# Optimization experiments

Hardware: AMD Instinct MI355X
Metric: run time of the kernel (lower is better)

Reference implementation:

```python
import jax, jax.numpy as jnp
import numpy as np

B, T, H = 1024, 1024, 64


def _lstm_cell(x, h, c, w_ih, w_hh, b_ih, b_hh):
    # gates: [B, 4H] in PyTorch order i, f, g, o
    g = x @ w_ih.T + h @ w_hh.T + b_ih + b_hh
    i, f, gg, o = jnp.split(g, 4, axis=-1)
    i = jax.nn.sigmoid(i)
    f = jax.nn.sigmoid(f)
    gg = jnp.tanh(gg)
    o = jax.nn.sigmoid(o)
    c_new = f * c + i * gg
    h_new = o * jnp.tanh(c_new)
    return h_new, c_new


def setup_inputs() -> dict:
    key = jax.random.key(0)
    ks = jax.random.split(key, 12)
    s = 1.0 / np.sqrt(H)  # torch default init scale
    r = lambda k, shape: jax.random.normal(k, shape, dtype=jnp.float32) * s
    return {
        "x": jax.random.normal(ks[0], (B, T), dtype=jnp.float32),
        "w_ih1": r(ks[1], (4 * H, 1)),
        "w_hh1": r(ks[2], (4 * H, H)),
        "b_ih1": r(ks[3], (4 * H,)),
        "b_hh1": r(ks[4], (4 * H,)),
        "w_ih2": r(ks[5], (4 * H, H)),
        "w_hh2": r(ks[6], (4 * H, H)),
        "b_ih2": r(ks[7], (4 * H,)),
        "b_hh2": r(ks[8], (4 * H,)),
        "w_lin": r(ks[9], (1, H)),
        "b_lin": r(ks[10], (1,)),
        "future_preds": 0,
    }


def reference(x, w_ih1, w_hh1, b_ih1, b_hh1, w_ih2, w_hh2, b_ih2, b_hh2,
              w_lin, b_lin, future_preds):
    bsz = x.shape[0]
    h1 = jnp.zeros((bsz, H), x.dtype)
    c1 = jnp.zeros((bsz, H), x.dtype)
    h2 = jnp.zeros((bsz, H), x.dtype)
    c2 = jnp.zeros((bsz, H), x.dtype)

    def step(carry, x_t):
        h1, c1, h2, c2 = carry
        h1, c1 = _lstm_cell(x_t, h1, c1, w_ih1, w_hh1, b_ih1, b_hh1)
        h2, c2 = _lstm_cell(h1, h2, c2, w_ih2, w_hh2, b_ih2, b_hh2)
        out = h2 @ w_lin.T + b_lin  # [B, 1]
        return (h1, c1, h2, c2), out

    xs = x.T[:, :, None]  # [T, B, 1]
    carry, outs = jax.lax.scan(step, (h1, c1, h2, c2), xs)
    outputs = outs[:, :, 0].T  # [B, T]

    if future_preds > 0:
        last = outs[-1]  # [B, 1]

        def fstep(carry, _):
            h1, c1, h2, c2, prev = carry
            h1, c1 = _lstm_cell(prev, h1, c1, w_ih1, w_hh1, b_ih1, b_hh1)
            h2, c2 = _lstm_cell(h1, h2, c2, w_ih2, w_hh2, b_ih2, b_hh2)
            out = h2 @ w_lin.T + b_lin
            return (h1, c1, h2, c2, out), out

        _, fouts = jax.lax.scan(fstep, (*carry, last), None, length=future_preds)
        outputs = jnp.concatenate([outputs, fouts[:, :, 0].T], axis=1)

    return outputs
```

## Files before the change

kernel.cpp:

```cpp
#include <hip/hip_runtime.h>
#include <hip/hip_bf16.h>


typedef _Float16 f16x8 __attribute__((ext_vector_type(8)));
typedef float    f32x4 __attribute__((ext_vector_type(4)));

namespace {
constexpr int Bb = 1024;
constexpr int Tt = 1024;
constexpr int NBat = 4;
constexpr int HSTR = 72;
constexpr int XSTR = 1025;

__device__ __forceinline__ int srow(int row) {
    return row ^ ((row >> 3) & 7);
}
__device__ __forceinline__ float sigm_pre(float a) {
    return __builtin_amdgcn_rcpf(1.0f + __builtin_amdgcn_exp2f(a));
}
__device__ __forceinline__ float tanh_pre(float a) {
    return fmaf(2.0f, __builtin_amdgcn_rcpf(1.0f + __builtin_amdgcn_exp2f(a)), -1.0f);
}
__device__ __forceinline__ float tanh_f(float x) {
    float e = __builtin_amdgcn_exp2f(-2.8853900817779268f * x);
    return fmaf(2.0f, __builtin_amdgcn_rcpf(1.0f + e), -1.0f);
}
template <int CTRL>
__device__ __forceinline__ float dpp_sum_step(float p) {
    int v = __builtin_amdgcn_update_dpp(0, __float_as_int(p), CTRL, 0xf, 0xf, true);
    return p + __int_as_float(v);
}
__device__ __forceinline__ bool detect_f32(const void* w) {
    const unsigned short* p = (const unsigned short*)w;
    int sane = 0;
    for (int i = 0; i < 64; ++i) {
        int e = (p[2 * i] >> 7) & 0xFF;
        if (e >= 107 && e <= 129) ++sane;
    }
    return sane < 32;
}
__device__ __forceinline__ float ld(const void* p, int i, bool f32) {
    return f32 ? ((const float*)p)[i]
               : __bfloat162float(((const __hip_bfloat16*)p)[i]);
}
__device__ __forceinline__ void st(void* p, int i, float v, bool f32) {
    if (f32) ((float*)p)[i] = v;
    else     ((__hip_bfloat16*)p)[i] = __float2bfloat16(v);
}
__device__ __forceinline__ void poll_flags(const int* f, int tp, int tq, int lane) {
    const int idx = lane & 7;
    const int thr = (idx < 4) ? tp : tq;
    for (;;) {
        int v = ((const volatile int*)f)[idx];
        if (__all(v >= thr)) break;
    }
    __builtin_amdgcn_sched_barrier(0);
    asm volatile("" ::: "memory");
}
}

__global__ __launch_bounds__(512, 1) void lstm2_kernel(
    const void* __restrict__ x,
    const void* __restrict__ w_ih1,
    const void* __restrict__ w_hh1,
    const void* __restrict__ b_ih1,
    const void* __restrict__ b_hh1,
    const void* __restrict__ w_ih2,
    const void* __restrict__ w_hh2,
    const void* __restrict__ b_ih2,
    const void* __restrict__ b_hh2,
    const void* __restrict__ w_lin,
    const void* __restrict__ b_lin,
    void* __restrict__ out)
{
    const int tid  = threadIdx.x;
    const int lane = tid & 63;
    const int w    = tid >> 6;
    const int gw   = w & 3;
    const bool isP = w < 4;
    const int m    = lane & 15;
    const int quad = lane >> 4;
    const int bb   = blockIdx.x * NBat;

    const bool f32 = detect_f32(w_hh1);

    __shared__ float                  xs[NBat * XSTR];
    __shared__ __align__(16) _Float16 h1ring[4][16 * HSTR];
    __shared__ __align__(16) _Float16 h2buf[2][16 * HSTR];
    __shared__ __align__(16) float    scr1[4][64 * 4];
    __shared__ __align__(16) float    scr2[4][64 * 4];
    __shared__ float                  headl[2][16];
    __shared__ float                  outbuf[NBat * Tt];
    __shared__ int                    flg[8];

    for (int i = tid; i < NBat * 1024; i += 512)
        xs[(i >> 10) * XSTR + (i & 1023)] = ld(x, (bb + (i >> 10)) * Tt + (i & 1023), f32);
    for (int i = tid; i < 16 * HSTR; i += 512) {
        h1ring[0][i] = (_Float16)0; h1ring[1][i] = (_Float16)0;
        h1ring[2][i] = (_Float16)0; h1ring[3][i] = (_Float16)0;
        h2buf[0][i] = (_Float16)0;  h2buf[1][i] = (_Float16)0;
    }
    if (tid < 8) flg[tid] = 0;

    const int arow = lane & 15;
    const int g_ld = arow & 3;
    const int u_ld = arow >> 2;
    const float scA = (g_ld == 2) ? -2.8853900817779268f : -1.4426950408889634f;
    f16x8 wfA[4][2], wfB[4][2];
    {
        const void* MA = isP ? w_hh1 : w_ih2;
#pragma unroll
        for (int q = 0; q < 4; ++q) {
            const int row = 64 * g_ld + 16 * gw + 4 * q + u_ld;
#pragma unroll
            for (int s = 0; s < 2; ++s) {
                const int base = row * 64 + 32 * s + quad * 8;
                if (f32) {
                    const float* A = (const float*)MA;
                    const float* B = (const float*)w_hh2;
#pragma unroll
                    for (int j = 0; j < 8; ++j) {
                        wfA[q][s][j] = (_Float16)(scA * A[base + j]);
                        wfB[q][s][j] = isP ? (_Float16)0.0f
                                           : (_Float16)(scA * B[base + j]);
                    }
                } else {
                    const __hip_bfloat16* A = (const __hip_bfloat16*)MA;
                    const __hip_bfloat16* B = (const __hip_bfloat16*)w_hh2;
#pragma unroll
                    for (int j = 0; j < 8; ++j) {
                        wfA[q][s][j] = (_Float16)(scA * __bfloat162float(A[base + j]));
                        wfB[q][s][j] = isP ? (_Float16)0.0f
                                           : (_Float16)(scA * __bfloat162float(B[base + j]));
                    }
                }
            }
        }
    }
    f32x4 bv[4], wxv[4];
#pragma unroll
    for (int q = 0; q < 4; ++q)
#pragma unroll
        for (int r = 0; r < 4; ++r) {
            const int row = 64 * r + 16 * gw + 4 * q + quad;
            const float sg = (r == 2) ? -2.8853900817779268f : -1.4426950408889634f;
            bv[q][r] = sg * (isP ? (ld(b_ih1, row, f32) + ld(b_hh1, row, f32))
                                 : (ld(b_ih2, row, f32) + ld(b_hh2, row, f32)));
            wxv[q][r] = isP ? sg * ld(w_ih1, row, f32) : 0.0f;
        }
    const int cb = lane >> 4;
    const int uo = lane & 15;
    const int cidx = srow(lane) * 4;
    int swadr[4];
#pragma unroll
    for (int q = 0; q < 4; ++q) swadr[q] = srow(m * 16 + q * 4 + quad) * 4;
    const float wl_u = ld(w_lin, 16 * gw + uo, f32);
    const float blin = ld(b_lin, 0, f32);
    float cst = 0.0f;
    __syncthreads();

    if (isP) {
        f16x8 pa0{}, pa1{};
#pragma unroll 4
        for (int t = 0; t < Tt; ++t) {
            poll_flags(flg, t, t - 3, lane);
            f32x4 acc[4];
            const float xt = xs[(m & (NBat - 1)) * XSTR + t];
#pragma unroll
            for (int q = 0; q < 4; ++q)
#pragma unroll
                for (int r = 0; r < 4; ++r)
                    acc[q][r] = fmaf(xt, wxv[q][r], bv[q][r]);
            if (t > 0) {
                const _Float16* hp = h1ring[(t - 1) & 3] + m * HSTR;
                if (m < NBat) {
                    pa0 = *(const f16x8*)(hp + quad * 8);
                    pa1 = *(const f16x8*)(hp + 32 + quad * 8);
                }
                __builtin_amdgcn_s_setprio(1);
#pragma unroll
                for (int q = 0; q < 4; ++q) {
                    acc[q] = __builtin_amdgcn_mfma_f32_16x16x32_f16(wfA[q][0], pa0, acc[q], 0, 0, 0);
                    acc[q] = __builtin_amdgcn_mfma_f32_16x16x32_f16(wfA[q][1], pa1, acc[q], 0, 0, 0);
                }
                __builtin_amdgcn_s_setprio(0);
            }
            if (m < NBat)
#pragma unroll
                for (int q = 0; q < 4; ++q)
                    *(f32x4*)&scr1[gw][swadr[q]] = acc[q];
            const f32x4 g = *(const f32x4*)&scr1[gw][cidx];
            float ig = sigm_pre(g[0]), fg = sigm_pre(g[1]);
            float gg = tanh_pre(g[2]), og = sigm_pre(g[3]);
            cst = fmaf(fg, cst, ig * gg);
            h1ring[t & 3][cb * HSTR + 16 * gw + uo] = (_Float16)(og * tanh_f(cst));
            if (lane == 0) {
                asm volatile("" ::: "memory");
                *(volatile int*)&flg[gw] = t + 1;
            }
        }
    } else {
        f16x8 pa0{}, pa1{}, pb0{}, pb1{};
#pragma unroll 4
        for (int u = 0; u < Tt; ++u) {
            poll_flags(flg, u + 1, u, lane);
            if (u > 0 && w == 4 && lane < NBat) {
                float s = blin;
#pragma unroll
                for (int k = 0; k < 4; ++k) s += headl[(u - 1) & 1][k * 4 + lane];
                outbuf[lane * Tt + (u - 1)] = s;
            }
            const _Float16* h1p = h1ring[u & 3] + m * HSTR;
            const _Float16* h2p = h2buf[(u + 1) & 1] + m * HSTR;
            if (m < NBat) {
                pa0 = *(const f16x8*)(h1p + quad * 8);
                pa1 = *(const f16x8*)(h1p + 32 + quad * 8);
                pb0 = *(const f16x8*)(h2p + quad * 8);
                pb1 = *(const f16x8*)(h2p + 32 + quad * 8);
            }
            f32x4 acc[4];
            __builtin_amdgcn_s_setprio(1);
#pragma unroll
            for (int q = 0; q < 4; ++q) {
                f32x4 p2 = __builtin_amdgcn_mfma_f32_16x16x32_f16(wfA[q][0], pa0, bv[q], 0, 0, 0);
                p2 = __builtin_amdgcn_mfma_f32_16x16x32_f16(wfA[q][1], pa1, p2, 0, 0, 0);
                f32x4 p3 = __builtin_amdgcn_mfma_f32_16x16x32_f16(wfB[q][0], pb0, f32x4{0,0,0,0}, 0, 0, 0);
                p3 = __builtin_amdgcn_mfma_f32_16x16x32_f16(wfB[q][1], pb1, p3, 0, 0, 0);
                acc[q] = p2 + p3;
            }
            __builtin_amdgcn_s_setprio(0);
            if (m < NBat)
#pragma unroll
                for (int q = 0; q < 4; ++q)
                    *(f32x4*)&scr2[gw][swadr[q]] = acc[q];
            const f32x4 g = *(const f32x4*)&scr2[gw][cidx];
            float ig = sigm_pre(g[0]), fg = sigm_pre(g[1]);
            float gg = tanh_pre(g[2]), og = sigm_pre(g[3]);
            cst = fmaf(fg, cst, ig * gg);
            float h = og * tanh_f(cst);
            h2buf[u & 1][cb * HSTR + 16 * gw + uo] = (_Float16)h;
            float p = h * wl_u;
            p = dpp_sum_step<0x111>(p);
            p = dpp_sum_step<0x112>(p);
            p = dpp_sum_step<0x114>(p);
            p = dpp_sum_step<0x118>(p);
            if (uo == 15) headl[u & 1][gw * 4 + cb] = p;
            if (lane == 0) {
                asm volatile("" ::: "memory");
                *(volatile int*)&flg[4 + gw] = u + 1;
            }
        }
        if (w == 4) {
            poll_flags(flg, 0, Tt, lane);
            if (lane < NBat) {
                float s = blin;
#pragma unroll
                for (int k = 0; k < 4; ++k) s += headl[(Tt - 1) & 1][k * 4 + lane];
                outbuf[lane * Tt + (Tt - 1)] = s;
            }
        }
    }
    __syncthreads();
    for (int i = tid; i < NBat * Tt; i += 512)
        st(out, (bb + (i >> 10)) * Tt + (i & 1023), outbuf[i], f32);
}

extern "C" void kernel_launch(void* const* d_in, const int* in_sizes, int n_in,
                              void* d_out, int out_size, void* d_ws, size_t ws_size,
                              hipStream_t stream)
{
    (void)in_sizes; (void)n_in; (void)out_size; (void)d_ws; (void)ws_size;
    lstm2_kernel<<<dim3(Bb / NBat), dim3(512), 0, stream>>>(
        d_in[0], d_in[1], d_in[2], d_in[3], d_in[4], d_in[5],
        d_in[6], d_in[7], d_in[8], d_in[9], d_in[10], d_out);
}
```

Baseline: 757.8 us.

## Compute LSTM gates directly in MFMA output registers, dropping LDS scratch transpose

Each lane now applies the gate nonlinearities and cell update to its four MFMA accumulator vectors in place, instead of writing them to an LDS scratch buffer and reading them back transposed. Every lane keeps four cell states, and only lanes for valid batch rows write h. The linear head becomes a per-lane FMA partial sum stored to LDS, replacing the DPP reduction. MFMA accumulation chains are split into independent products that are summed afterwards, and the layer-1 input projection is hoisted above the flag poll. The cost is 4x redundant transcendental work per lane, since 12 of the 16 MFMA columns are padding.

```diff
diff --git a/kernel.cpp b/kernel.cpp
--- a/kernel.cpp
+++ b/kernel.cpp
@@ -12,9 +12,6 @@
 constexpr int HSTR = 72;
 constexpr int XSTR = 1025;
 
-__device__ __forceinline__ int srow(int row) {
-    return row ^ ((row >> 3) & 7);
-}
 __device__ __forceinline__ float sigm_pre(float a) {
     return __builtin_amdgcn_rcpf(1.0f + __builtin_amdgcn_exp2f(a));
 }
@@ -24,11 +21,6 @@
 __device__ __forceinline__ float tanh_f(float x) {
     float e = __builtin_amdgcn_exp2f(-2.8853900817779268f * x);
     return fmaf(2.0f, __builtin_amdgcn_rcpf(1.0f + e), -1.0f);
-}
-template <int CTRL>
-__device__ __forceinline__ float dpp_sum_step(float p) {
-    int v = __builtin_amdgcn_update_dpp(0, __float_as_int(p), CTRL, 0xf, 0xf, true);
-    return p + __int_as_float(v);
 }
 __device__ __forceinline__ bool detect_f32(const void* w) {
     const unsigned short* p = (const unsigned short*)w;
@@ -87,9 +79,7 @@
     __shared__ float                  xs[NBat * XSTR];
     __shared__ __align__(16) _Float16 h1ring[4][16 * HSTR];
     __shared__ __align__(16) _Float16 h2buf[2][16 * HSTR];
-    __shared__ __align__(16) float    scr1[4][64 * 4];
-    __shared__ __align__(16) float    scr2[4][64 * 4];
-    __shared__ float                  headl[2][16];
+    __shared__ __align__(16) float    headp[2][NBat][16];
     __shared__ float                  outbuf[NBat * Tt];
     __shared__ int                    flg[8];
 
@@ -148,29 +138,27 @@
                                  : (ld(b_ih2, row, f32) + ld(b_hh2, row, f32)));
             wxv[q][r] = isP ? sg * ld(w_ih1, row, f32) : 0.0f;
         }
-    const int cb = lane >> 4;
-    const int uo = lane & 15;
-    const int cidx = srow(lane) * 4;
-    int swadr[4];
-#pragma unroll
-    for (int q = 0; q < 4; ++q) swadr[q] = srow(m * 16 + q * 4 + quad) * 4;
-    const float wl_u = ld(w_lin, 16 * gw + uo, f32);
+    float wlv[4];
+#pragma unroll
+    for (int q = 0; q < 4; ++q) wlv[q] = ld(w_lin, 16 * gw + 4 * q + quad, f32);
     const float blin = ld(b_lin, 0, f32);
-    float cst = 0.0f;
+    const int hwbase = m * HSTR + 16 * gw + quad;
+    float cst[4] = {0.0f, 0.0f, 0.0f, 0.0f};
     __syncthreads();
 
     if (isP) {
         f16x8 pa0{}, pa1{};
 #pragma unroll 4
         for (int t = 0; t < Tt; ++t) {
+            const float xt = xs[(m & (NBat - 1)) * XSTR + t];
+            f32x4 ai[4];
+#pragma unroll
+            for (int q = 0; q < 4; ++q)
+#pragma unroll
+                for (int r = 0; r < 4; ++r)
+                    ai[q][r] = fmaf(xt, wxv[q][r], bv[q][r]);
             poll_flags(flg, t, t - 3, lane);
             f32x4 acc[4];
-            const float xt = xs[(m & (NBat - 1)) * XSTR + t];
-#pragma unroll
-            for (int q = 0; q < 4; ++q)
-#pragma unroll
-                for (int r = 0; r < 4; ++r)
-                    acc[q][r] = fmaf(xt, wxv[q][r], bv[q][r]);
             if (t > 0) {
                 const _Float16* hp = h1ring[(t - 1) & 3] + m * HSTR;
                 if (m < NBat) {
@@ -180,20 +168,28 @@
                 __builtin_amdgcn_s_setprio(1);
 #pragma unroll
                 for (int q = 0; q < 4; ++q) {
-                    acc[q] = __builtin_amdgcn_mfma_f32_16x16x32_f16(wfA[q][0], pa0, acc[q], 0, 0, 0);
-                    acc[q] = __builtin_amdgcn_mfma_f32_16x16x32_f16(wfA[q][1], pa1, acc[q], 0, 0, 0);
+                    f32x4 p0 = __builtin_amdgcn_mfma_f32_16x16x32_f16(wfA[q][0], pa0, ai[q], 0, 0, 0);
+                    f32x4 p1 = __builtin_amdgcn_mfma_f32_16x16x32_f16(wfA[q][1], pa1, f32x4{0,0,0,0}, 0, 0, 0);
+                    acc[q] = p0 + p1;
                 }
                 __builtin_amdgcn_s_setprio(0);
-            }
-            if (m < NBat)
-#pragma unroll
-                for (int q = 0; q < 4; ++q)
-                    *(f32x4*)&scr1[gw][swadr[q]] = acc[q];
-            const f32x4 g = *(const f32x4*)&scr1[gw][cidx];
-            float ig = sigm_pre(g[0]), fg = sigm_pre(g[1]);
-            float gg = tanh_pre(g[2]), og = sigm_pre(g[3]);
-            cst = fmaf(fg, cst, ig * gg);
-            h1ring[t & 3][cb * HSTR + 16 * gw + uo] = (_Float16)(og * tanh_f(cst));
+            } else {
+#pragma unroll
+                for (int q = 0; q < 4; ++q) acc[q] = ai[q];
+            }
+            _Float16 hq[4];
+#pragma unroll
+            for (int q = 0; q < 4; ++q) {
+                float ig = sigm_pre(acc[q][0]), fg = sigm_pre(acc[q][1]);
+                float gg = tanh_pre(acc[q][2]), og = sigm_pre(acc[q][3]);
+                cst[q] = fmaf(fg, cst[q], ig * gg);
+                hq[q] = (_Float16)(og * tanh_f(cst[q]));
+            }
+            if (m < NBat) {
+                _Float16* hw = h1ring[t & 3] + hwbase;
+#pragma unroll
+                for (int q = 0; q < 4; ++q) hw[4 * q] = hq[q];
+            }
             if (lane == 0) {
                 asm volatile("" ::: "memory");
                 *(volatile int*)&flg[gw] = t + 1;
@@ -205,10 +201,13 @@
         for (int u = 0; u < Tt; ++u) {
             poll_flags(flg, u + 1, u, lane);
             if (u > 0 && w == 4 && lane < NBat) {
-                float s = blin;
-#pragma unroll
-                for (int k = 0; k < 4; ++k) s += headl[(u - 1) & 1][k * 4 + lane];
-                outbuf[lane * Tt + (u - 1)] = s;
+                const float* hp2 = &headp[(u - 1) & 1][lane][0];
+                f32x4 s0 = *(const f32x4*)(hp2);
+                f32x4 s1 = *(const f32x4*)(hp2 + 4);
+                f32x4 s2 = *(const f32x4*)(hp2 + 8);
+                f32x4 s3 = *(const f32x4*)(hp2 + 12);
+                f32x4 sv = (s0 + s1) + (s2 + s3);
+                outbuf[lane * Tt + (u - 1)] = blin + (sv[0] + sv[1]) + (sv[2] + sv[3]);
             }
             const _Float16* h1p = h1ring[u & 3] + m * HSTR;
             const _Float16* h2p = h2buf[(u + 1) & 1] + m * HSTR;
@@ -222,29 +221,31 @@
             __builtin_amdgcn_s_setprio(1);
 #pragma unroll
             for (int q = 0; q < 4; ++q) {
-                f32x4 p2 = __builtin_amdgcn_mfma_f32_16x16x32_f16(wfA[q][0], pa0, bv[q], 0, 0, 0);
-                p2 = __builtin_amdgcn_mfma_f32_16x16x32_f16(wfA[q][1], pa1, p2, 0, 0, 0);
-                f32x4 p3 = __builtin_amdgcn_mfma_f32_16x16x32_f16(wfB[q][0], pb0, f32x4{0,0,0,0}, 0, 0, 0);
-                p3 = __builtin_amdgcn_mfma_f32_16x16x32_f16(wfB[q][1], pb1, p3, 0, 0, 0);
-                acc[q] = p2 + p3;
+                f32x4 p0 = __builtin_amdgcn_mfma_f32_16x16x32_f16(wfA[q][0], pa0, bv[q], 0, 0, 0);
+                f32x4 p1 = __builtin_amdgcn_mfma_f32_16x16x32_f16(wfA[q][1], pa1, f32x4{0,0,0,0}, 0, 0, 0);
+                f32x4 p2 = __builtin_amdgcn_mfma_f32_16x16x32_f16(wfB[q][0], pb0, f32x4{0,0,0,0}, 0, 0, 0);
+                f32x4 p3 = __builtin_amdgcn_mfma_f32_16x16x32_f16(wfB[q][1], pb1, f32x4{0,0,0,0}, 0, 0, 0);
+                acc[q] = (p0 + p1) + (p2 + p3);
             }
             __builtin_amdgcn_s_setprio(0);
-            if (m < NBat)
-#pragma unroll
-                for (int q = 0; q < 4; ++q)
-                    *(f32x4*)&scr2[gw][swadr[q]] = acc[q];
-            const f32x4 g = *(const f32x4*)&scr2[gw][cidx];
-            float ig = sigm_pre(g[0]), fg = sigm_pre(g[1]);
-            float gg = tanh_pre(g[2]), og = sigm_pre(g[3]);
-            cst = fmaf(fg, cst, ig * gg);
-            float h = og * tanh_f(cst);
-            h2buf[u & 1][cb * HSTR + 16 * gw + uo] = (_Float16)h;
-            float p = h * wl_u;
-            p = dpp_sum_step<0x111>(p);
-            p = dpp_sum_step<0x112>(p);
-            p = dpp_sum_step<0x114>(p);
-            p = dpp_sum_step<0x118>(p);
-            if (uo == 15) headl[u & 1][gw * 4 + cb] = p;
+            float hq[4];
+#pragma unroll
+            for (int q = 0; q < 4; ++q) {
+                float ig = sigm_pre(acc[q][0]), fg = sigm_pre(acc[q][1]);
+                float gg = tanh_pre(acc[q][2]), og = sigm_pre(acc[q][3]);
+                cst[q] = fmaf(fg, cst[q], ig * gg);
+                hq[q] = og * tanh_f(cst[q]);
+            }
+            if (m < NBat) {
+                _Float16* hw = h2buf[u & 1] + hwbase;
+#pragma unroll
+                for (int q = 0; q < 4; ++q) hw[4 * q] = (_Float16)hq[q];
+                float p = hq[0] * wlv[0];
+                p = fmaf(hq[1], wlv[1], p);
+                p = fmaf(hq[2], wlv[2], p);
+                p = fmaf(hq[3], wlv[3], p);
+                headp[u & 1][m][gw * 4 + quad] = p;
+            }
             if (lane == 0) {
                 asm volatile("" ::: "memory");
                 *(volatile int*)&flg[4 + gw] = u + 1;
@@ -253,10 +254,13 @@
         if (w == 4) {
             poll_flags(flg, 0, Tt, lane);
             if (lane < NBat) {
-                float s = blin;
-#pragma unroll
-                for (int k = 0; k < 4; ++k) s += headl[(Tt - 1) & 1][k * 4 + lane];
-                outbuf[lane * Tt + (Tt - 1)] = s;
+                const float* hp2 = &headp[(Tt - 1) & 1][lane][0];
+                f32x4 s0 = *(const f32x4*)(hp2);
+                f32x4 s1 = *(const f32x4*)(hp2 + 4);
+                f32x4 s2 = *(const f32x4*)(hp2 + 8);
+                f32x4 s3 = *(const f32x4*)(hp2 + 12);
+                f32x4 sv = (s0 + s1) + (s2 + s3);
+                outbuf[lane * Tt + (Tt - 1)] = blin + (sv[0] + sv[1]) + (sv[2] + sv[3]);
             }
         }
     }
```

New measurement: 1.056 ms. 1.39x slower.
